# Kernel tuning notes

Measured on AMD Instinct MI355X. Metric: run time of the kernel, lower is better.

The kernel has to match this reference:

```python
import jax, jax.numpy as jnp
import numpy as np


def _conv(x, w, b):
    # NCHW conv, SAME padding for odd kernel, stride 1
    pad = (w.shape[2] - 1) // 2
    y = jax.lax.conv_general_dilated(
        x, w, window_strides=(1, 1), padding=[(pad, pad), (pad, pad)],
        dimension_numbers=('NCHW', 'OIHW', 'NCHW'))
    return y + b[None, :, None, None]


def _cell(x, h, c, m, p):
    # one TransGRU cell step; x:[B,Cin,H,W], h/c/m:[B,hc,H,W]
    A = _conv(jnp.concatenate([x, h], axis=1), p['w_rzo'], p['b_rzo'])   # [B,3hc,H,W]
    Bm = _conv(jnp.concatenate([x, m], axis=1), p['w_rz'], p['b_rz'])    # [B,2hc,H,W]
    decay_h = jnp.exp(-p['td_h'])[None]          # (1,hc,1,1)
    decay_m = jnp.exp(-p['td_m'])[None]
    gate = jax.nn.sigmoid(p['tg'])[None]
    Ar, Az, Ao = jnp.split(A, 3, axis=1)
    Br, Bz = jnp.split(Bm, 2, axis=1)
    r = jax.nn.sigmoid(Ar * gate + h * decay_h)
    z = jax.nn.sigmoid(Az * gate + h * decay_h)
    o = jax.nn.sigmoid(Ao)
    xr = jax.nn.sigmoid(Br * gate + m * decay_m)
    xz = jax.nn.sigmoid(Bz * gate + m * decay_m)
    gc = jnp.tanh(_conv(jnp.concatenate([x, r * c], axis=1), p['w_h'], p['b_h']))
    gm = jnp.tanh(_conv(jnp.concatenate([x, xr * m], axis=1), p['w_h'], p['b_h']))
    c_new = z * c + (1 - z) * gc
    m_new = xz * m + (1 - xz) * gm
    h_new = o * jnp.tanh(_conv(jnp.concatenate([c_new, m_new], axis=1), p['w_o'], p['b_o']))
    return h_new, c_new, m_new, (r, z, xr, xz, c_new, m_new, gc, gm, o)


def _forward(x, params, attention_size):
    B, T, _, H, W = x.shape
    L = len(params)
    hcs = [p['w_rzo'].shape[0] // 3 for p in params]
    hc_last = hcs[-1]
    dtype = x.dtype
    init_states = tuple(
        tuple(jnp.zeros((B, hc, H, W), dtype) for _ in range(3)) for hc in hcs)
    init_gates = tuple(jnp.zeros((B, hc_last, H, W), dtype) for _ in range(9))

    def step(carry, xt):
        states, _ = carry
        inp = xt
        m = states[-1][2]  # layer 0 reads m from last layer of previous step
        new_states = []
        gates = None
        for l in range(L):
            h, c, _own_m = states[l]
            inp, cn, mn, gates = _cell(inp, h, c, m, params[l])
            new_states.append((inp, cn, mn))
            m = mn  # next layer reads m just produced by this layer
        return (tuple(new_states), gates), inp

    (final_states, gates), hs = jax.lax.scan(
        step, (init_states, init_gates), jnp.swapaxes(x, 0, 1))
    # gates from last layer at final step (matches torch leaking loop vars)
    r, z, xr, xz, c, m, gc, gm, o = gates
    q = ((r + xr + c + gc) * 0.25).reshape(B, hc_last, H * W)
    k = ((r + xr + m + gm) * 0.25).reshape(B, hc_last, H * W)
    v = jnp.swapaxes(hs, 0, 1).reshape(B, T, hc_last, H * W)
    scale = 1.0 / float(np.sqrt(attention_size))
    attn = jax.nn.softmax(jnp.einsum('bcn,bdn->bcd', q, k) * scale, axis=-1)
    out = jnp.einsum('bcd,btdn->btcn', attn, v).reshape(B, T, hc_last, H, W)
    return out


def setup_inputs() -> dict:
    key = jax.random.key(0)
    ks = jax.random.split(key, 32)
    d = {'x': jax.random.normal(ks[0], (4, 8, 16, 64, 64), jnp.float32)}
    specs = {
        'w_rzo0': (192, 80, 3, 3), 'b_rzo0': (192,), 'w_rz0': (128, 80, 3, 3),
        'b_rz0': (128,), 'w_h0': (64, 80, 3, 3), 'b_h0': (64,),
        'w_o0': (64, 128, 1, 1), 'b_o0': (64,), 'td_h0': (64, 1, 1),
        'td_m0': (64, 1, 1), 'tg0': (64, 1, 1),
        'w_rzo1': (192, 128, 3, 3), 'b_rzo1': (192,), 'w_rz1': (128, 128, 3, 3),
        'b_rz1': (128,), 'w_h1': (64, 128, 3, 3), 'b_h1': (64,),
        'w_o1': (64, 128, 1, 1), 'b_o1': (64,), 'td_h1': (64, 1, 1),
        'td_m1': (64, 1, 1), 'tg1': (64, 1, 1),
    }
    for i, (name, shp) in enumerate(specs.items()):
        d[name] = jax.random.normal(ks[i + 1], shp, jnp.float32) * 0.05
    d['attention_size'] = 4096
    return d


def reference(x, w_rzo0, b_rzo0, w_rz0, b_rz0, w_h0, b_h0, w_o0, b_o0,
              td_h0, td_m0, tg0, w_rzo1, b_rzo1, w_rz1, b_rz1, w_h1, b_h1,
              w_o1, b_o1, td_h1, td_m1, tg1, attention_size):
    params = [
        dict(w_rzo=w_rzo0, b_rzo=b_rzo0, w_rz=w_rz0, b_rz=b_rz0, w_h=w_h0,
             b_h=b_h0, w_o=w_o0, b_o=b_o0, td_h=td_h0, td_m=td_m0, tg=tg0),
        dict(w_rzo=w_rzo1, b_rzo=b_rzo1, w_rz=w_rz1, b_rz=b_rz1, w_h=w_h1,
             b_h=b_h1, w_o=w_o1, b_o=b_o1, td_h=td_h1, td_m=td_m1, tg=tg1),
    ]
    return _forward(x, params, attention_size)
```

## Files before the change

### kernel.cpp

```cpp
#include <hip/hip_runtime.h>
#include <math.h>

#define HWN 4096
#define Bn 4
#define Tn 8

typedef __attribute__((ext_vector_type(8))) _Float16 f16x8;
typedef __attribute__((ext_vector_type(4))) float floatx4;

__device__ __forceinline__ float sigmoidf_(float v) { return 1.f / (1.f + expf(-v)); }

__device__ __forceinline__ void split8(const float* vv, f16x8* hi, f16x8* lo) {
#pragma unroll
    for (int j = 0; j < 8; ++j) {
        _Float16 h = (_Float16)vv[j];
        (*hi)[j] = h;
        (*lo)[j] = (_Float16)(vv[j] - (float)h);
    }
}

__global__ __launch_bounds__(256) void prep_w_kernel(
    const float* __restrict__ W, _Float16* __restrict__ dst,
    int Ctot, int Cout, int nch, int KK)
{
    const int ncog = Cout >> 4;
    const long total = (long)KK * nch * ncog * 512;
    for (long i = (long)blockIdx.x * 256 + threadIdx.x; i < total;
         i += (long)gridDim.x * 256) {
        int j    = (int)(i & 7);
        int lane = (int)((i >> 3) & 63);
        long r   = i >> 9;
        int f = (int)(r % ncog); r /= ncog;
        int c = (int)(r % nch);  r /= nch;
        int kk = (int)r;
        int co = f * 16 + (lane & 15);
        int ci = c * 32 + (lane >> 4) * 8 + j;
        float v = (ci < Ctot) ? W[((long)co * Ctot + ci) * KK + kk] : 0.f;
        _Float16 hi = (_Float16)v;
        dst[i]         = hi;
        dst[total + i] = (_Float16)(v - (float)hi);
    }
}

__global__ __launch_bounds__(256) void prep_x_kernel(
    const float* __restrict__ x, float* __restrict__ xcl)
{
    const int i = blockIdx.x * 256 + threadIdx.x;
    const int px = i & 4095;
    const int t  = (i >> 12) & 7;
    const int b  = i >> 15;
    float* d = xcl + (((long)t * Bn + b) * HWN + px) * 16;
#pragma unroll
    for (int ch = 0; ch < 16; ++ch)
        d[ch] = x[((long)(b * 8 + t) * 16 + ch) * HWN + px];
}

template<int EPI, int NF, int TR>
__global__ __launch_bounds__(256) void conv3m(
    const float* __restrict__ in1, int C1,
    const float* __restrict__ in2a, const float* __restrict__ in2b,
    int Ctot, int nch,
    const _Float16* __restrict__ wA, const float* __restrict__ biasA,
    float* outA, int CoutA, int ncogA,
    const _Float16* __restrict__ wB, const float* __restrict__ biasB,
    float* outB, int CoutB, int ncogB, int nA,
    const float* zA, const float* zB,
    const float* sA, const float* sB,
    const float* rten, const float* xrten,
    float* qout, float* kout, int last)
{
    constexpr int G = TR / 4;
    constexpr int SLOTS = (TR + 2) * 18 * 4;
    constexpr int NS = (SLOTS + 255) / 256;
    __shared__ __align__(16) _Float16 ldsB[TR + 2][18][2][40];

    const int tid = threadIdx.x;
    const int ty0 = (blockIdx.x >> 2) * TR;
    const int tx0 = (blockIdx.x & 3) * 16;
    const int b   = blockIdx.z & 3;
    const int which = (EPI == 1) ? (int)(blockIdx.z >> 2)
                                 : (blockIdx.y >= (unsigned)nA ? 1 : 0);

    const float*    in2  = which ? in2b : in2a;
    const _Float16* Wf   = which ? wB : wA;
    const float*    bias = which ? biasB : biasA;
    float*          outp = which ? outB : outA;
    const int Cout = which ? CoutB : CoutA;
    const int ncog = which ? ncogB : ncogA;
    const int cog0 = (EPI == 1) ? blockIdx.y * NF
                   : (which ? (blockIdx.y - nA) * NF : blockIdx.y * NF);
    const int co0  = cog0 * 16;

    const int lane = tid & 63, wv = tid >> 6, tl = lane & 15, quad = lane >> 4;
    const int C2 = Ctot - C1;
    const long wplane = (long)9 * nch * ncog * 512;
    const float* in1b  = in1 + (long)b * HWN * C1;
    const float* in2bb = in2 + (long)b * HWN * C2;

    floatx4 acc[NF][G];
#pragma unroll
    for (int f = 0; f < NF; ++f)
#pragma unroll
        for (int g = 0; g < G; ++g) acc[f][g] = (floatx4){0.f, 0.f, 0.f, 0.f};

    float4 pa[NS], pb[NS];
    auto prefetch = [&](int c) {
        const int c0 = c * 32;
#pragma unroll
        for (int s = 0; s < NS; ++s) {
            const int i = tid + s * 256;
            float4 va = {0.f, 0.f, 0.f, 0.f}, vb = {0.f, 0.f, 0.f, 0.f};
            if (i < SLOTS) {
                const int pxh = i >> 2, cig = i & 3;
                const int yh = pxh / 18, xh = pxh - yh * 18;
                const int y = ty0 + yh - 1, x = tx0 + xh - 1;
                const int ch = c0 + cig * 8;
                if (ch < Ctot && (unsigned)y < 64u && (unsigned)x < 64u) {
                    const float* src; long off;
                    if (ch < C1) { src = in1b;  off = (long)(y * 64 + x) * C1 + ch; }
                    else         { src = in2bb; off = (long)(y * 64 + x) * C2 + ch - C1; }
                    va = *(const float4*)(src + off);
                    vb = *(const float4*)(src + off + 4);
                }
            }
            pa[s] = va; pb[s] = vb;
        }
    };

    prefetch(0);

    for (int c = 0; c < nch; ++c) {
        f16x8 wh[5][NF], wl[5][NF];
#define LOADW(S, BUF)                                                           \
        {                                                                       \
            const int kk_ = ((S) % 3) * 3 + (S) / 3;                            \
            const long wo_ = ((long)(kk_ * nch + c) * ncog + cog0) * 512 + lane * 8; \
            _Pragma("unroll")                                                   \
            for (int f = 0; f < NF; ++f) {                                      \
                wh[BUF][f] = *(const f16x8*)(Wf + wo_ + (long)f * 512);         \
                wl[BUF][f] = *(const f16x8*)(Wf + wplane + wo_ + (long)f * 512);\
            }                                                                   \
        }
        LOADW(0, 0)
        LOADW(1, 1)
        LOADW(2, 2)
        LOADW(3, 3)

        __syncthreads();
#pragma unroll
        for (int s = 0; s < NS; ++s) {
            const int i = tid + s * 256;
            if (i < SLOTS) {
                const int pxh = i >> 2, cig = i & 3;
                const int yh = pxh / 18, xh = pxh - yh * 18;
                float vv[8] = {pa[s].x, pa[s].y, pa[s].z, pa[s].w,
                               pb[s].x, pb[s].y, pb[s].z, pb[s].w};
                f16x8 vh, vl;
                split8(vv, &vh, &vl);
                *(f16x8*)&ldsB[yh][xh][0][cig * 8] = vh;
                *(f16x8*)&ldsB[yh][xh][1][cig * 8] = vl;
            }
        }
        __syncthreads();

#pragma unroll
        for (int kx = 0; kx < 3; ++kx) {
            f16x8 rh[G + 2], rl[G + 2];
#pragma unroll
            for (int rr = 0; rr < G + 2; ++rr) {
                const _Float16* pB = &ldsB[wv * G + rr][tl + kx][0][quad * 8];
                rh[rr] = *(const f16x8*)pB;
                rl[rr] = *(const f16x8*)(pB + 40);
            }
#pragma unroll
            for (int ky = 0; ky < 3; ++ky) {
                const int s = kx * 3 + ky;
                if (s < 5) LOADW(s + 4, (s + 4) % 5)
                const int cur = s % 5;
#pragma unroll
                for (int f = 0; f < NF; ++f)
#pragma unroll
                    for (int g = 0; g < G; ++g) {
                        acc[f][g] = __builtin_amdgcn_mfma_f32_16x16x32_f16(wh[cur][f], rh[g + ky], acc[f][g], 0, 0, 0);
                        acc[f][g] = __builtin_amdgcn_mfma_f32_16x16x32_f16(wh[cur][f], rl[g + ky], acc[f][g], 0, 0, 0);
                        acc[f][g] = __builtin_amdgcn_mfma_f32_16x16x32_f16(wl[cur][f], rh[g + ky], acc[f][g], 0, 0, 0);
                    }
            }
            if (kx == 1 && c + 1 < nch) prefetch(c + 1);
        }
#undef LOADW
    }

    if (EPI == 0) {
        const long obb = (long)b * HWN * Cout;
#pragma unroll
        for (int f = 0; f < NF; ++f) {
            const int co = co0 + f * 16 + quad * 4;
#pragma unroll
            for (int g = 0; g < G; ++g) {
                const long px = (long)(ty0 + wv * G + g) * 64 + tx0 + tl;
                float4 v;
                v.x = acc[f][g][0] + bias[co + 0];
                v.y = acc[f][g][1] + bias[co + 1];
                v.z = acc[f][g][2] + bias[co + 2];
                v.w = acc[f][g][3] + bias[co + 3];
                *(float4*)(outp + obb + px * Cout + co) = v;
            }
        }
    } else {
        const float* zt = which ? zB : zA;
        const float* st = which ? sB : sA;
        float* qk = which ? kout : qout;
#pragma unroll
        for (int f = 0; f < NF; ++f) {
            const int co = co0 + f * 16 + quad * 4;
#pragma unroll
            for (int g = 0; g < G; ++g) {
                const long px = (long)(ty0 + wv * G + g) * 64 + tx0 + tl;
                const long off = (long)b * HWN * 64 + px * 64 + co;
                float4 zv = *(const float4*)(zt + off);
                float4 sv = *(const float4*)(st + off);
                float gv[4], cn[4];
                gv[0] = tanhf(acc[f][g][0] + bias[co + 0]);
                gv[1] = tanhf(acc[f][g][1] + bias[co + 1]);
                gv[2] = tanhf(acc[f][g][2] + bias[co + 2]);
                gv[3] = tanhf(acc[f][g][3] + bias[co + 3]);
                cn[0] = zv.x * sv.x + (1.f - zv.x) * gv[0];
                cn[1] = zv.y * sv.y + (1.f - zv.y) * gv[1];
                cn[2] = zv.z * sv.z + (1.f - zv.z) * gv[2];
                cn[3] = zv.w * sv.w + (1.f - zv.w) * gv[3];
                *(float4*)(outp + off) = *(float4*)cn;
                if (last) {
                    float4 rv = *(const float4*)(rten + off);
                    float4 xv = *(const float4*)(xrten + off);
                    qk[((long)(b * 64) + co + 0) * HWN + px] = 0.25f * (rv.x + xv.x + cn[0] + gv[0]);
                    qk[((long)(b * 64) + co + 1) * HWN + px] = 0.25f * (rv.y + xv.y + cn[1] + gv[1]);
                    qk[((long)(b * 64) + co + 2) * HWN + px] = 0.25f * (rv.z + xv.z + cn[2] + gv[2]);
                    qk[((long)(b * 64) + co + 3) * HWN + px] = 0.25f * (rv.w + xv.w + cn[3] + gv[3]);
                }
            }
        }
    }
}

__global__ __launch_bounds__(256) void conv1x1m(
    const float* __restrict__ cten, const float* __restrict__ mten,
    const float* __restrict__ oten,
    const _Float16* __restrict__ W, const float* __restrict__ bias,
    float* houtp)
{
    const int tid = threadIdx.x;
    const int lane = tid & 63, wv = tid >> 6, tl = lane & 15, quad = lane >> 4;
    const int b = blockIdx.y;
    const int fh = blockIdx.x & 1;
    const int px = (blockIdx.x >> 1) * 64 + wv * 16 + tl;
    const long bb = (long)b * HWN * 64;

    f16x8 wh[4][2], wl[4][2];
#pragma unroll
    for (int c = 0; c < 4; ++c)
#pragma unroll
        for (int f = 0; f < 2; ++f) {
            const long wo = (long)(c * 4 + fh * 2 + f) * 512 + lane * 8;
            wh[c][f] = *(const f16x8*)(W + wo);
            wl[c][f] = *(const f16x8*)(W + 8192 + wo);
        }
    f16x8 bh[4], bl[4];
#pragma unroll
    for (int c = 0; c < 4; ++c) {
        const float* src = (c < 2) ? cten : mten;
        const int ch0 = (c & 1) * 32 + quad * 8;
        const long off = bb + (long)px * 64 + ch0;
        float4 p0 = *(const float4*)(src + off);
        float4 p1 = *(const float4*)(src + off + 4);
        float vv[8] = {p0.x, p0.y, p0.z, p0.w, p1.x, p1.y, p1.z, p1.w};
        split8(vv, &bh[c], &bl[c]);
    }

    floatx4 acc[2];
#pragma unroll
    for (int f = 0; f < 2; ++f) acc[f] = (floatx4){0.f, 0.f, 0.f, 0.f};
#pragma unroll
    for (int c = 0; c < 4; ++c)
#pragma unroll
        for (int f = 0; f < 2; ++f) {
            acc[f] = __builtin_amdgcn_mfma_f32_16x16x32_f16(wh[c][f], bh[c], acc[f], 0, 0, 0);
            acc[f] = __builtin_amdgcn_mfma_f32_16x16x32_f16(wh[c][f], bl[c], acc[f], 0, 0, 0);
            acc[f] = __builtin_amdgcn_mfma_f32_16x16x32_f16(wl[c][f], bh[c], acc[f], 0, 0, 0);
        }

#pragma unroll
    for (int f = 0; f < 2; ++f) {
        const int co = fh * 32 + f * 16 + quad * 4;
        const long off = bb + (long)px * 64 + co;
        float4 ov = *(const float4*)(oten + off);
        float4 hv;
        hv.x = ov.x * tanhf(acc[f][0] + bias[co + 0]);
        hv.y = ov.y * tanhf(acc[f][1] + bias[co + 1]);
        hv.z = ov.z * tanhf(acc[f][2] + bias[co + 2]);
        hv.w = ov.w * tanhf(acc[f][3] + bias[co + 3]);
        *(float4*)(houtp + off) = hv;
    }
}

__global__ __launch_bounds__(256) void gates_cl(
    const float* __restrict__ A, const float* __restrict__ Bm,
    const float* __restrict__ h, const float* __restrict__ m,
    const float* __restrict__ c,
    const float* __restrict__ td_h, const float* __restrict__ td_m,
    const float* __restrict__ tg,
    float* r, float* xr, float* z, float* xz,
    float* o, float* rc, float* xm, int write_r)
{
    const int i  = blockIdx.x * 256 + threadIdx.x;
    const int ch = (i & 15) * 4;
    const long px = (i >> 4) & 4095;
    const int b  = i >> 16;
    const long b64  = ((long)b * HWN + px) * 64 + ch;
    const long b192 = ((long)b * HWN + px) * 192 + ch;
    const long b128 = ((long)b * HWN + px) * 128 + ch;

    float4 Ar = *(const float4*)(A + b192);
    float4 Az = *(const float4*)(A + b192 + 64);
    float4 Ao = *(const float4*)(A + b192 + 128);
    float4 Br = *(const float4*)(Bm + b128);
    float4 Bz = *(const float4*)(Bm + b128 + 64);
    float4 hv = *(const float4*)(h + b64);
    float4 mv = *(const float4*)(m + b64);
    float4 cv = *(const float4*)(c + b64);

    float rv[4], zv[4], ov[4], xrv[4], xzv[4], rcv[4], xmv[4];
    const float* Arp = (const float*)&Ar; const float* Azp = (const float*)&Az;
    const float* Aop = (const float*)&Ao; const float* Brp = (const float*)&Br;
    const float* Bzp = (const float*)&Bz; const float* hp = (const float*)&hv;
    const float* mp = (const float*)&mv;  const float* cp = (const float*)&cv;
#pragma unroll
    for (int j = 0; j < 4; ++j) {
        const float g  = sigmoidf_(tg[ch + j]);
        const float dh = expf(-td_h[ch + j]);
        const float dm = expf(-td_m[ch + j]);
        rv[j]  = sigmoidf_(Arp[j] * g + hp[j] * dh);
        zv[j]  = sigmoidf_(Azp[j] * g + hp[j] * dh);
        ov[j]  = sigmoidf_(Aop[j]);
        xrv[j] = sigmoidf_(Brp[j] * g + mp[j] * dm);
        xzv[j] = sigmoidf_(Bzp[j] * g + mp[j] * dm);
        rcv[j] = rv[j] * cp[j];
        xmv[j] = xrv[j] * mp[j];
    }
    if (write_r) {
        *(float4*)(r  + b64) = *(float4*)rv;
        *(float4*)(xr + b64) = *(float4*)xrv;
    }
    *(float4*)(z  + b64) = *(float4*)zv;
    *(float4*)(xz + b64) = *(float4*)xzv;
    *(float4*)(o  + b64) = *(float4*)ov;
    *(float4*)(rc + b64) = *(float4*)rcv;
    *(float4*)(xm + b64) = *(float4*)xmv;
}

__global__ __launch_bounds__(256) void logits_part(
    const float* __restrict__ q, const float* __restrict__ k, float* __restrict__ part)
{
    __shared__ float qs[64][66], ks[64][66];
    const int tid = threadIdx.x;
    const int b = blockIdx.x, kc = blockIdx.y;
    const int cqq = tid >> 4, ckq = tid & 15;
    float pacc[4][4];
#pragma unroll
    for (int u = 0; u < 4; ++u)
#pragma unroll
        for (int v = 0; v < 4; ++v) pacc[u][v] = 0.f;

    for (int sub = 0; sub < 4; ++sub) {
        const int px0 = kc * 256 + sub * 64;
        __syncthreads();
#pragma unroll
        for (int rr = 0; rr < 16; ++rr) {
            const int idx = rr * 256 + tid;
            const int chh = idx >> 6, pxo = idx & 63;
            qs[chh][pxo] = q[((long)b * 64 + chh) * HWN + px0 + pxo];
            ks[chh][pxo] = k[((long)b * 64 + chh) * HWN + px0 + pxo];
        }
        __syncthreads();
        for (int p = 0; p < 64; ++p) {
            float qv[4], kv[4];
#pragma unroll
            for (int u = 0; u < 4; ++u) { qv[u] = qs[cqq + 16 * u][p]; kv[u] = ks[ckq + 16 * u][p]; }
#pragma unroll
            for (int u = 0; u < 4; ++u)
#pragma unroll
                for (int v = 0; v < 4; ++v) pacc[u][v] = fmaf(qv[u], kv[v], pacc[u][v]);
        }
    }
#pragma unroll
    for (int u = 0; u < 4; ++u)
#pragma unroll
        for (int v = 0; v < 4; ++v)
            part[(((long)b * 16 + kc) * 64 + cqq + 16 * u) * 64 + ckq + 16 * v] = pacc[u][v];
}

__global__ void reduce_softmax(const float* __restrict__ part, float* __restrict__ attn)
{
    const int row = blockIdx.x;
    const int b = row >> 6, cq = row & 63;
    const int lane = threadIdx.x;
    float s = 0.f;
#pragma unroll
    for (int kc = 0; kc < 16; ++kc)
        s += part[(((long)b * 16 + kc) * 64 + cq) * 64 + lane];
    float v = s * (1.f / 64.f);
    float mx = v;
    for (int off = 32; off; off >>= 1) mx = fmaxf(mx, __shfl_xor(mx, off));
    float e = expf(v - mx);
    float sum = e;
    for (int off = 32; off; off >>= 1) sum += __shfl_xor(sum, off);
    attn[row * 64 + lane] = e / sum;
}

__global__ __launch_bounds__(256) void out_cl(
    const float* __restrict__ attn, const float* __restrict__ hs,
    float* __restrict__ outp)
{
    __shared__ __align__(16) float att_t[64][8];
    const int bt = blockIdx.x;
    const int b = bt >> 3, t = bt & 7;
    const int c0 = blockIdx.z * 8;
    const int tid = threadIdx.x;
    for (int i = tid; i < 512; i += 256) {
        int d = i >> 3, j = i & 7;
        att_t[d][j] = attn[(b * 64 + c0 + j) * 64 + d];
    }
    __syncthreads();

    const long px = blockIdx.y * 256 + tid;
    const long SLOT = (long)Bn * HWN * 64;
    const float* vb = hs + (long)t * SLOT + ((long)b * HWN + px) * 64;

    float acc[8];
#pragma unroll
    for (int j = 0; j < 8; ++j) acc[j] = 0.f;
#pragma unroll 4
    for (int dg = 0; dg < 16; ++dg) {
        float4 v4 = *(const float4*)(vb + dg * 4);
        const float* vp = (const float*)&v4;
#pragma unroll
        for (int j4 = 0; j4 < 4; ++j4) {
            const float vv = vp[j4];
            const float4 a0 = *(const float4*)&att_t[dg * 4 + j4][0];
            const float4 a1 = *(const float4*)&att_t[dg * 4 + j4][4];
            acc[0] = fmaf(vv, a0.x, acc[0]); acc[1] = fmaf(vv, a0.y, acc[1]);
            acc[2] = fmaf(vv, a0.z, acc[2]); acc[3] = fmaf(vv, a0.w, acc[3]);
            acc[4] = fmaf(vv, a1.x, acc[4]); acc[5] = fmaf(vv, a1.y, acc[5]);
            acc[6] = fmaf(vv, a1.z, acc[6]); acc[7] = fmaf(vv, a1.w, acc[7]);
        }
    }
    const long ob = ((long)(b * 8 + t) * 64 + c0) * HWN + px;
#pragma unroll
    for (int j = 0; j < 8; ++j) outp[ob + (long)j * HWN] = acc[j];
}

extern "C" void kernel_launch(void* const* d_in, const int* in_sizes, int n_in,
                              void* d_out, int out_size, void* d_ws, size_t ws_size,
                              hipStream_t stream)
{
    const float* x = (const float*)d_in[0];
    const float* w_rzo[2] = {(const float*)d_in[1],  (const float*)d_in[12]};
    const float* b_rzo[2] = {(const float*)d_in[2],  (const float*)d_in[13]};
    const float* w_rz[2]  = {(const float*)d_in[3],  (const float*)d_in[14]};
    const float* b_rz[2]  = {(const float*)d_in[4],  (const float*)d_in[15]};
    const float* w_h[2]   = {(const float*)d_in[5],  (const float*)d_in[16]};
    const float* b_h[2]   = {(const float*)d_in[6],  (const float*)d_in[17]};
    const float* w_o[2]   = {(const float*)d_in[7],  (const float*)d_in[18]};
    const float* b_o[2]   = {(const float*)d_in[8],  (const float*)d_in[19]};
    const float* td_h[2]  = {(const float*)d_in[9],  (const float*)d_in[20]};
    const float* td_m[2]  = {(const float*)d_in[10], (const float*)d_in[21]};
    const float* tg[2]    = {(const float*)d_in[11], (const float*)d_in[22]};

    const size_t S64 = (size_t)Bn * HWN * 64;
    float* P = (float*)d_ws;
    float* h0    = P; P += S64;
    float* c0    = P; P += S64;
    float* m0    = P; P += S64;
    float* c1    = P; P += S64;
    float* m1    = P; P += S64;
    float* zslab = P; P += S64;
    float* A_cl  = P; P += (size_t)Bn * HWN * 192;
    float* B_cl  = P; P += (size_t)Bn * HWN * 128;
    float* rb    = P; P += S64;
    float* xrb   = P; P += S64;
    float* zb    = P; P += S64;
    float* xzb   = P; P += S64;
    float* ogb   = P; P += S64;
    float* rcb   = P; P += S64;
    float* xmb   = P; P += S64;
    float* hs    = P; P += (size_t)Tn * S64;
    float* x_cl  = P; P += (size_t)Tn * Bn * HWN * 16;
    _Float16* wA0 = (_Float16*)P;
    _Float16* wB0 = wA0 + 331776;
    _Float16* wH0 = wB0 + 221184;
    _Float16* wA1 = wH0 + 110592;
    _Float16* wB1 = wA1 + 442368;
    _Float16* wH1 = wB1 + 294912;
    _Float16* wO0 = wH1 + 147456;
    _Float16* wO1 = wO0 + 16384;
    float* qbuf  = A_cl;
    float* kbuf  = qbuf + S64;
    float* partb = kbuf + S64;
    float* attnb = partb + (size_t)Bn * 16 * 64 * 64;

    hipMemsetAsync(h0, 0, 6 * S64 * sizeof(float), stream);

    prep_x_kernel<<<512, 256, 0, stream>>>(x, x_cl);
    prep_w_kernel<<<128, 256, 0, stream>>>(w_rzo[0], wA0, 80, 192, 3, 9);
    prep_w_kernel<<<128, 256, 0, stream>>>(w_rz[0],  wB0, 80, 128, 3, 9);
    prep_w_kernel<<<128, 256, 0, stream>>>(w_h[0],   wH0, 80,  64, 3, 9);
    prep_w_kernel<<<128, 256, 0, stream>>>(w_rzo[1], wA1, 128, 192, 4, 9);
    prep_w_kernel<<<128, 256, 0, stream>>>(w_rz[1],  wB1, 128, 128, 4, 9);
    prep_w_kernel<<<128, 256, 0, stream>>>(w_h[1],   wH1, 128, 64, 4, 9);
    prep_w_kernel<<<64, 256, 0, stream>>>(w_o[0], wO0, 128, 64, 4, 1);
    prep_w_kernel<<<64, 256, 0, stream>>>(w_o[1], wO1, 128, 64, 4, 1);

    for (int t = 0; t < Tn; ++t) {
        const float* xt = x_cl + (size_t)t * Bn * HWN * 16;
        const float* h1prev = (t == 0) ? zslab : (hs + (size_t)(t - 1) * S64);
        float* h1out = hs + (size_t)t * S64;
        const int lastq = (t == Tn - 1) ? 1 : 0;

        conv3m<0, 2, 16><<<dim3(16, 10, 4), 256, 0, stream>>>(
            xt, 16, h0, m1, 80, 3,
            wA0, b_rzo[0], A_cl, 192, 12,
            wB0, b_rz[0],  B_cl, 128, 8, 6,
            nullptr, nullptr, nullptr, nullptr, nullptr, nullptr, nullptr, nullptr, 0);
        gates_cl<<<1024, 256, 0, stream>>>(A_cl, B_cl, h0, m1, c0,
            td_h[0], td_m[0], tg[0], rb, xrb, zb, xzb, ogb, rcb, xmb, 0);
        conv3m<1, 2, 8><<<dim3(32, 2, 8), 256, 0, stream>>>(
            xt, 16, rcb, xmb, 80, 3,
            wH0, b_h[0], c0, 64, 4,
            wH0, b_h[0], m0, 64, 4, 0,
            zb, xzb, c0, m1, rb, xrb, qbuf, kbuf, 0);
        conv1x1m<<<dim3(128, 4), 256, 0, stream>>>(c0, m0, ogb, wO0, b_o[0], h0);

        conv3m<0, 2, 16><<<dim3(16, 10, 4), 256, 0, stream>>>(
            h0, 64, h1prev, m0, 128, 4,
            wA1, b_rzo[1], A_cl, 192, 12,
            wB1, b_rz[1],  B_cl, 128, 8, 6,
            nullptr, nullptr, nullptr, nullptr, nullptr, nullptr, nullptr, nullptr, 0);
        gates_cl<<<1024, 256, 0, stream>>>(A_cl, B_cl, h1prev, m0, c1,
            td_h[1], td_m[1], tg[1], rb, xrb, zb, xzb, ogb, rcb, xmb, lastq);
        conv3m<1, 2, 8><<<dim3(32, 2, 8), 256, 0, stream>>>(
            h0, 64, rcb, xmb, 128, 4,
            wH1, b_h[1], c1, 64, 4,
            wH1, b_h[1], m1, 64, 4, 0,
            zb, xzb, c1, m0, rb, xrb, qbuf, kbuf, lastq);
        conv1x1m<<<dim3(128, 4), 256, 0, stream>>>(c1, m1, ogb, wO1, b_o[1], h1out);
    }

    logits_part<<<dim3(4, 16), 256, 0, stream>>>(qbuf, kbuf, partb);
    reduce_softmax<<<256, 64, 0, stream>>>(partb, attnb);
    out_cl<<<dim3(32, 16, 8), 256, 0, stream>>>(attnb, hs, (float*)d_out);
}
```

Before: 1.331 ms.

## Fuse gate activations into rzo/rz conv epilogue and retile candidate conv

Removes the separate gates kernel. The first 3x3 conv epilogue now applies the sigmoid gates with precomputed decay and gate constants and writes r*c, xr*m, z, xz, o and r/xr directly, so the A/B pre-activation buffers are no longer written and read back. The constants come from a tiny prep kernel that stores them in the now-unused B_cl buffer. The candidate conv is also relaunched with NF=1, TR=16 and a different grid shape. This saves one launch per layer-step and a large round-trip of intermediate traffic, at the cost of a heavier conv epilogue and repurposed argument slots.

New measurement: 1.314 ms. About the same (-1.2%).

```diff
diff --git a/kernel.cpp b/kernel.cpp
--- a/kernel.cpp
+++ b/kernel.cpp
@@ -55,6 +55,15 @@
         d[ch] = x[((long)(b * 8 + t) * 16 + ch) * HWN + px];
 }
 
+__global__ void prep_gc(const float* __restrict__ tg, const float* __restrict__ tdh,
+                        const float* __restrict__ tdm, float* __restrict__ gc)
+{
+    const int j = threadIdx.x;
+    gc[j]       = sigmoidf_(tg[j]);
+    gc[64 + j]  = expf(-tdh[j]);
+    gc[128 + j] = expf(-tdm[j]);
+}
+
 template<int EPI, int NF, int TR>
 __global__ __launch_bounds__(256) void conv3m(
     const float* __restrict__ in1, int C1,
@@ -64,10 +73,9 @@
     float* outA, int CoutA, int ncogA,
     const _Float16* __restrict__ wB, const float* __restrict__ biasB,
     float* outB, int CoutB, int ncogB, int nA,
-    const float* zA, const float* zB,
-    const float* sA, const float* sB,
-    const float* rten, const float* xrten,
-    float* qout, float* kout, int last)
+    float* s1, float* s2, float* s3, float* s4,
+    float* s5, float* s6, float* s7, float* s8,
+    const float* __restrict__ gc, int last)
 {
     constexpr int G = TR / 4;
     constexpr int SLOTS = (TR + 2) * 18 * 4;
@@ -192,25 +200,65 @@
     }
 
     if (EPI == 0) {
-        const long obb = (long)b * HWN * Cout;
+        const int gid = co0 >> 6;
+        const long bb64 = (long)b * HWN * 64;
+        const float* dec = which ? in2b : in2a;
+        const float* cs  = (const float*)s8;
+        float* g0   = which ? s2 : s1;
+        float* g1   = which ? s4 : s3;
+        float* rout = which ? s7 : s6;
 #pragma unroll
         for (int f = 0; f < NF; ++f) {
             const int co = co0 + f * 16 + quad * 4;
+            const int ch = co & 63;
+            float gvc[4], dvc[4];
+            if (gid < 2) {
+#pragma unroll
+                for (int j = 0; j < 4; ++j) {
+                    gvc[j] = gc[ch + j];
+                    dvc[j] = gc[(which ? 128 : 64) + ch + j];
+                }
+            }
 #pragma unroll
             for (int g = 0; g < G; ++g) {
                 const long px = (long)(ty0 + wv * G + g) * 64 + tx0 + tl;
-                float4 v;
-                v.x = acc[f][g][0] + bias[co + 0];
-                v.y = acc[f][g][1] + bias[co + 1];
-                v.z = acc[f][g][2] + bias[co + 2];
-                v.w = acc[f][g][3] + bias[co + 3];
-                *(float4*)(outp + obb + px * Cout + co) = v;
+                const long off = bb64 + px * 64 + ch;
+                float vv[4];
+                vv[0] = acc[f][g][0] + bias[co + 0];
+                vv[1] = acc[f][g][1] + bias[co + 1];
+                vv[2] = acc[f][g][2] + bias[co + 2];
+                vv[3] = acc[f][g][3] + bias[co + 3];
+                if (gid == 2) {
+                    float ov[4];
+#pragma unroll
+                    for (int j = 0; j < 4; ++j) ov[j] = sigmoidf_(vv[j]);
+                    *(float4*)(s5 + off) = *(float4*)ov;
+                } else {
+                    float4 dv = *(const float4*)(dec + off);
+                    const float* dvp = (const float*)&dv;
+                    float rr[4];
+#pragma unroll
+                    for (int j = 0; j < 4; ++j)
+                        rr[j] = sigmoidf_(vv[j] * gvc[j] + dvp[j] * dvc[j]);
+                    if (gid == 0) {
+                        float4 sv = dv;
+                        if (!which) sv = *(const float4*)(cs + off);
+                        const float* svp = (const float*)&sv;
+                        float outv[4];
+#pragma unroll
+                        for (int j = 0; j < 4; ++j) outv[j] = rr[j] * svp[j];
+                        *(float4*)(g0 + off) = *(float4*)outv;
+                        if (last) *(float4*)(rout + off) = *(float4*)rr;
+                    } else {
+                        *(float4*)(g1 + off) = *(float4*)rr;
+                    }
+                }
             }
         }
     } else {
-        const float* zt = which ? zB : zA;
-        const float* st = which ? sB : sA;
-        float* qk = which ? kout : qout;
+        const float* zt = which ? s2 : s1;
+        const float* st = which ? s4 : s3;
+        float* qk = which ? s8 : s7;
 #pragma unroll
         for (int f = 0; f < NF; ++f) {
             const int co = co0 + f * 16 + quad * 4;
@@ -231,8 +279,8 @@
                 cn[3] = zv.w * sv.w + (1.f - zv.w) * gv[3];
                 *(float4*)(outp + off) = *(float4*)cn;
                 if (last) {
-                    float4 rv = *(const float4*)(rten + off);
-                    float4 xv = *(const float4*)(xrten + off);
+                    float4 rv = *(const float4*)(s5 + off);
+                    float4 xv = *(const float4*)(s6 + off);
                     qk[((long)(b * 64) + co + 0) * HWN + px] = 0.25f * (rv.x + xv.x + cn[0] + gv[0]);
                     qk[((long)(b * 64) + co + 1) * HWN + px] = 0.25f * (rv.y + xv.y + cn[1] + gv[1]);
                     qk[((long)(b * 64) + co + 2) * HWN + px] = 0.25f * (rv.z + xv.z + cn[2] + gv[2]);
@@ -301,61 +349,6 @@
         hv.w = ov.w * tanhf(acc[f][3] + bias[co + 3]);
         *(float4*)(houtp + off) = hv;
     }
-}
-
-__global__ __launch_bounds__(256) void gates_cl(
-    const float* __restrict__ A, const float* __restrict__ Bm,
-    const float* __restrict__ h, const float* __restrict__ m,
-    const float* __restrict__ c,
-    const float* __restrict__ td_h, const float* __restrict__ td_m,
-    const float* __restrict__ tg,
-    float* r, float* xr, float* z, float* xz,
-    float* o, float* rc, float* xm, int write_r)
-{
-    const int i  = blockIdx.x * 256 + threadIdx.x;
-    const int ch = (i & 15) * 4;
-    const long px = (i >> 4) & 4095;
-    const int b  = i >> 16;
-    const long b64  = ((long)b * HWN + px) * 64 + ch;
-    const long b192 = ((long)b * HWN + px) * 192 + ch;
-    const long b128 = ((long)b * HWN + px) * 128 + ch;
-
-    float4 Ar = *(const float4*)(A + b192);
-    float4 Az = *(const float4*)(A + b192 + 64);
-    float4 Ao = *(const float4*)(A + b192 + 128);
-    float4 Br = *(const float4*)(Bm + b128);
-    float4 Bz = *(const float4*)(Bm + b128 + 64);
-    float4 hv = *(const float4*)(h + b64);
-    float4 mv = *(const float4*)(m + b64);
-    float4 cv = *(const float4*)(c + b64);
-
-    float rv[4], zv[4], ov[4], xrv[4], xzv[4], rcv[4], xmv[4];
-    const float* Arp = (const float*)&Ar; const float* Azp = (const float*)&Az;
-    const float* Aop = (const float*)&Ao; const float* Brp = (const float*)&Br;
-    const float* Bzp = (const float*)&Bz; const float* hp = (const float*)&hv;
-    const float* mp = (const float*)&mv;  const float* cp = (const float*)&cv;
-#pragma unroll
-    for (int j = 0; j < 4; ++j) {
-        const float g  = sigmoidf_(tg[ch + j]);
-        const float dh = expf(-td_h[ch + j]);
-        const float dm = expf(-td_m[ch + j]);
-        rv[j]  = sigmoidf_(Arp[j] * g + hp[j] * dh);
-        zv[j]  = sigmoidf_(Azp[j] * g + hp[j] * dh);
-        ov[j]  = sigmoidf_(Aop[j]);
-        xrv[j] = sigmoidf_(Brp[j] * g + mp[j] * dm);
-        xzv[j] = sigmoidf_(Bzp[j] * g + mp[j] * dm);
-        rcv[j] = rv[j] * cp[j];
-        xmv[j] = xrv[j] * mp[j];
-    }
-    if (write_r) {
-        *(float4*)(r  + b64) = *(float4*)rv;
-        *(float4*)(xr + b64) = *(float4*)xrv;
-    }
-    *(float4*)(z  + b64) = *(float4*)zv;
-    *(float4*)(xz + b64) = *(float4*)xzv;
-    *(float4*)(o  + b64) = *(float4*)ov;
-    *(float4*)(rc + b64) = *(float4*)rcv;
-    *(float4*)(xm + b64) = *(float4*)xmv;
 }
 
 __global__ __launch_bounds__(256) void logits_part(
@@ -507,10 +500,14 @@
     float* kbuf  = qbuf + S64;
     float* partb = kbuf + S64;
     float* attnb = partb + (size_t)Bn * 16 * 64 * 64;
+    float* gc0   = B_cl;
+    float* gc1   = B_cl + 192;
 
     hipMemsetAsync(h0, 0, 6 * S64 * sizeof(float), stream);
 
     prep_x_kernel<<<512, 256, 0, stream>>>(x, x_cl);
+    prep_gc<<<1, 64, 0, stream>>>(tg[0], td_h[0], td_m[0], gc0);
+    prep_gc<<<1, 64, 0, stream>>>(tg[1], td_h[1], td_m[1], gc1);
     prep_w_kernel<<<128, 256, 0, stream>>>(w_rzo[0], wA0, 80, 192, 3, 9);
     prep_w_kernel<<<128, 256, 0, stream>>>(w_rz[0],  wB0, 80, 128, 3, 9);
     prep_w_kernel<<<128, 256, 0, stream>>>(w_h[0],   wH0, 80,  64, 3, 9);
@@ -528,30 +525,30 @@
 
         conv3m<0, 2, 16><<<dim3(16, 10, 4), 256, 0, stream>>>(
             xt, 16, h0, m1, 80, 3,
-            wA0, b_rzo[0], A_cl, 192, 12,
-            wB0, b_rz[0],  B_cl, 128, 8, 6,
-            nullptr, nullptr, nullptr, nullptr, nullptr, nullptr, nullptr, nullptr, 0);
-        gates_cl<<<1024, 256, 0, stream>>>(A_cl, B_cl, h0, m1, c0,
-            td_h[0], td_m[0], tg[0], rb, xrb, zb, xzb, ogb, rcb, xmb, 0);
-        conv3m<1, 2, 8><<<dim3(32, 2, 8), 256, 0, stream>>>(
+            wA0, b_rzo[0], nullptr, 192, 12,
+            wB0, b_rz[0],  nullptr, 128, 8, 6,
+            rcb, xmb, zb, xzb, ogb, rb, xrb, c0,
+            gc0, 0);
+        conv3m<1, 1, 16><<<dim3(16, 4, 8), 256, 0, stream>>>(
             xt, 16, rcb, xmb, 80, 3,
             wH0, b_h[0], c0, 64, 4,
             wH0, b_h[0], m0, 64, 4, 0,
-            zb, xzb, c0, m1, rb, xrb, qbuf, kbuf, 0);
+            zb, xzb, c0, m1, rb, xrb, qbuf, kbuf,
+            nullptr, 0);
         conv1x1m<<<dim3(128, 4), 256, 0, stream>>>(c0, m0, ogb, wO0, b_o[0], h0);
 
         conv3m<0, 2, 16><<<dim3(16, 10, 4), 256, 0, stream>>>(
             h0, 64, h1prev, m0, 128, 4,
-            wA1, b_rzo[1], A_cl, 192, 12,
-            wB1, b_rz[1],  B_cl, 128, 8, 6,
-            nullptr, nullptr, nullptr, nullptr, nullptr, nullptr, nullptr, nullptr, 0);
-        gates_cl<<<1024, 256, 0, stream>>>(A_cl, B_cl, h1prev, m0, c1,
-            td_h[1], td_m[1], tg[1], rb, xrb, zb, xzb, ogb, rcb, xmb, lastq);
-        conv3m<1, 2, 8><<<dim3(32, 2, 8), 256, 0, stream>>>(
+            wA1, b_rzo[1], nullptr, 192, 12,
+            wB1, b_rz[1],  nullptr, 128, 8, 6,
+            rcb, xmb, zb, xzb, ogb, rb, xrb, c1,
+            gc1, lastq);
+        conv3m<1, 1, 16><<<dim3(16, 4, 8), 256, 0, stream>>>(
             h0, 64, rcb, xmb, 128, 4,
             wH1, b_h[1], c1, 64, 4,
             wH1, b_h[1], m1, 64, 4, 0,
-            zb, xzb, c1, m0, rb, xrb, qbuf, kbuf, lastq);
+            zb, xzb, c1, m0, rb, xrb, qbuf, kbuf,
+            nullptr, lastq);
         conv1x1m<<<dim3(128, 4), 256, 0, stream>>>(c1, m1, ogb, wO1, b_o[1], h1out);
     }
 
```
